# Kernel tuning notes

Measured on AMD Instinct MI355X. Metric: run time of the kernel, lower is better.

## Reference

```python
import jax, jax.numpy as jnp
import numpy as np

HEAD_SIZE = 64
EMBED = 512


def setup_inputs() -> dict:
    key = jax.random.key(0)
    kx, kk, kq, kv = jax.random.split(key, 4)
    x = jax.random.normal(kx, (4, 4096, EMBED), dtype=jnp.float32)
    # torch Linear(EMBED, HEAD_SIZE, bias=False) weight: [HEAD_SIZE, EMBED]
    scale = 1.0 / np.sqrt(EMBED)
    Wk = jax.random.normal(kk, (HEAD_SIZE, EMBED), dtype=jnp.float32) * scale
    Wq = jax.random.normal(kq, (HEAD_SIZE, EMBED), dtype=jnp.float32) * scale
    Wv = jax.random.normal(kv, (HEAD_SIZE, EMBED), dtype=jnp.float32) * scale
    return {"x": x, "Wk": Wk, "Wq": Wq, "Wv": Wv}


def reference(x, Wk, Wq, Wv):
    B, T, C = x.shape
    # projections: x @ W.T  -> [B, T, H]
    k = jnp.einsum('btc,hc->bth', x, Wk)
    q = jnp.einsum('btc,hc->bth', x, Wq)
    v = jnp.einsum('btc,hc->bth', x, Wv)
    # scores scaled by C**-0.5 (input embed dim, as in the source module)
    scores = jnp.einsum('bth,bsh->bts', q, k) * (C ** -0.5)  # [B, T, T]
    causal = jnp.tril(jnp.ones((T, T), dtype=bool))
    scores = jnp.where(causal, scores, -jnp.inf)
    weights = jax.nn.softmax(scores, axis=-1)
    # dropout p=0.0 -> identity
    out = jnp.einsum('bts,bsh->bth', weights, v)  # [B, T, H]
    return out
```

## Files before the change

kernel.cpp:

```cpp
#include <hip/hip_runtime.h>

typedef unsigned short u16;
typedef unsigned int   u32;

#define NB 4
#define NT 4096
#define NC 512
#define NH 64
#define ATT_SCALE 0.044194173824159216f
#define LOG2E     1.4426950408889634f
#define QSCALE    (ATT_SCALE * LOG2E)
#define NEG_BIG   -30000.0f
#define ITEMS3_PB 288

typedef __attribute__((ext_vector_type(8))) _Float16 half8;
typedef __attribute__((ext_vector_type(4))) _Float16 half4;
typedef __attribute__((ext_vector_type(4))) float    floatx4;

__device__ __forceinline__ void gld16(const void* g, void* l) {
    __builtin_amdgcn_global_load_lds(
        (const __attribute__((address_space(1))) void*)g,
        (__attribute__((address_space(3))) void*)l, 16, 0, 0);
}


__global__ __launch_bounds__(256) void wconv(
    const float* __restrict__ Wk, const float* __restrict__ Wq,
    const float* __restrict__ Wv, _Float16* __restrict__ Wh)
{
    const int gid = blockIdx.x * 256 + threadIdx.x;
    const int w = gid >> 13;
    const int i = gid & 8191;
    const int h = i >> 7, c = (i & 127) * 4;
    const float* src = (w == 0) ? Wq : (w == 1) ? Wk : Wv;
    const float sc = (w == 0) ? QSCALE : 1.0f;
    float4 f = *(const float4*)&src[h * NC + c];
    half4 o = {(_Float16)(f.x * sc), (_Float16)(f.y * sc),
               (_Float16)(f.z * sc), (_Float16)(f.w * sc)};
    const int blk = ((w * 16 + (c >> 5)) * 4 + (h >> 4));
    *(half4*)&Wh[(size_t)blk * 512 + (h & 15) * 32 + ((c >> 3) & 3) * 8 + (c & 7)] = o;
}

__global__ __launch_bounds__(256) void qkv_mfma(
    const float* __restrict__ x, const _Float16* __restrict__ Wh,
    _Float16* __restrict__ Qf, _Float16* __restrict__ Kf,
    _Float16* __restrict__ Vf)
{
    __shared__ __align__(16) _Float16 Ws[2][12 * 512];
    __shared__ __align__(16) float    Xs[3][64 * 32];

    const int tid  = threadIdx.x;
    const int wv   = tid >> 6;
    const int lane = tid & 63;
    const int quad = lane >> 4;
    const int id   = lane & 15;
    const int loff = id * 32 + quad * 8;
    const int rowbase = blockIdx.x * 64;

    const int xrow  = wv * 16 + (lane >> 3);
    const int xchk  = (lane & 7) ^ ((lane >> 3) & 7);
    const float* xs0 = x + (size_t)(rowbase + xrow) * NC + xchk * 4;
    const float* xs1 = xs0 + 8 * NC;

    floatx4 acc[3][4] = {};

    gld16(xs0, &Xs[0][wv * 512]);
    gld16(xs1, &Xs[0][wv * 512 + 256]);
#pragma unroll
    for (int jj = 0; jj < 3; ++jj) {
        const int f = 3 * wv + jj;
        gld16(Wh + (size_t)(((f >> 2) * 16 + 0) * 4 + (f & 3)) * 512 + loff,
              &Ws[0][f * 512]);
    }
    gld16(xs0 + 32, &Xs[1][wv * 512]);
    gld16(xs1 + 32, &Xs[1][wv * 512 + 256]);

    int xcur = 0;
    for (int s = 0; s < 16; ++s) {
        if (s + 2 < 16) asm volatile("s_waitcnt vmcnt(2)" ::: "memory");
        else            asm volatile("s_waitcnt vmcnt(0)" ::: "memory");
        __syncthreads();

        if (s + 1 < 16) {
            _Float16* wdst = &Ws[(s + 1) & 1][0];
#pragma unroll
            for (int jj = 0; jj < 3; ++jj) {
                const int f = 3 * wv + jj;
                gld16(Wh + (size_t)(((f >> 2) * 16 + (s + 1)) * 4 + (f & 3)) * 512 + loff,
                      wdst + f * 512);
            }
        }
        if (s + 2 < 16) {
            const int nb = (xcur + 2 >= 3) ? xcur - 1 : xcur + 2;
            float* xdst = &Xs[nb][wv * 512];
            gld16(xs0 + (s + 2) * 32, xdst);
            gld16(xs1 + (s + 2) * 32, xdst + 256);
        }

        const float* Xc = &Xs[xcur][wv * 512 + id * 32];
        float4 f0 = *(const float4*)&Xc[((quad * 2 + 0) ^ (id & 7)) << 2];
        float4 f1 = *(const float4*)&Xc[((quad * 2 + 1) ^ (id & 7)) << 2];
        half8 a;
        a[0] = (_Float16)f0.x; a[1] = (_Float16)f0.y;
        a[2] = (_Float16)f0.z; a[3] = (_Float16)f0.w;
        a[4] = (_Float16)f1.x; a[5] = (_Float16)f1.y;
        a[6] = (_Float16)f1.z; a[7] = (_Float16)f1.w;

        const _Float16* Wc = &Ws[s & 1][0];
#pragma unroll
        for (int f = 0; f < 12; ++f) {
            half8 bf = *(const half8*)&Wc[f * 512 + lane * 8];
            acc[f >> 2][f & 3] = __builtin_amdgcn_mfma_f32_16x16x32_f16(a, bf, acc[f >> 2][f & 3], 0, 0, 0);
        }
        xcur = (xcur + 1 == 3) ? 0 : xcur + 1;
    }

    const int rowb = rowbase + wv * 16;
    const int b2 = rowb >> 12, L = rowb & 4095;
    const int q16 = L >> 4, ktt = L >> 6, tt = (L >> 4) & 3;
    const int kop = ((rowb & 63) + quad * 4) >> 5;
    const int q4k = (((rowb & 63) + quad * 4) >> 3) & 3;
#pragma unroll
    for (int nt = 0; nt < 4; ++nt) {
        const int hop = nt >> 1;
        const int q4h = (nt * 2 + (id >> 3)) & 3;
        const int j   = id & 7;
        const size_t qa2 = (size_t)((b2 * 256 + q16) * 2 + hop) * 512 + q4h * 8 + j;
        const size_t ka2 = (size_t)(((b2 * 64 + ktt) * 4 + tt) * 2 + hop) * 512 + q4h * 8 + j;
#pragma unroll
        for (int r = 0; r < 4; ++r) {
            Qf[qa2 + (quad * 4 + r) * 32] = (_Float16)acc[0][nt][r];
            Kf[ka2 + (quad * 4 + r) * 32] = (_Float16)acc[1][nt][r];
        }
        half4 vh = {(_Float16)acc[2][nt][0], (_Float16)acc[2][nt][1],
                    (_Float16)acc[2][nt][2], (_Float16)acc[2][nt][3]};
        const size_t va2 = (size_t)(((b2 * 64 + ktt) * 4 + nt) * 2 + kop) * 512
                         + id * 32 + q4k * 8 + (quad & 1) * 4;
        *(half4*)&Vf[va2] = vh;
    }
}

__global__ __launch_bounds__(256) void attn_part(
    const _Float16* __restrict__ Qf, const _Float16* __restrict__ Kf,
    const _Float16* __restrict__ Vf, _Float16* __restrict__ Opart,
    float2* __restrict__ MLpart)
{
    constexpr int KP = 72;
    __shared__ __align__(16) _Float16 KV[2][2][4096];
    __shared__ __align__(16) _Float16 Ps[4][16 * KP];

    const int tid  = threadIdx.x;
    const int wv   = tid >> 6;
    const int lane = tid & 63;
    const int quad = lane >> 4;
    const int id   = lane & 15;
    const int b    = blockIdx.y;
    const int item = (ITEMS3_PB - 1) - blockIdx.x;
    const int loff = id * 32 + quad * 8;

    int g = (int)(0.5f * (__builtin_sqrtf((float)item + 1.0f) - 1.0f));
    while (4 * (g + 1) * (g + 2) <= item) ++g;
    while (g > 0 && 4 * g * (g + 1) > item) --g;
    const int rem = item - 4 * g * (g + 1);
    const int np  = g + 1;
    const int qb  = 8 * g + rem / np;
    const int seg = rem - (rem / np) * np;
    const int ntl = qb + 1;
    const int t0 = seg * ntl / np, t1 = (seg + 1) * ntl / np;

    const size_t qa = (size_t)((b * 256 + qb * 4 + wv) * 2) * 512 + loff;
    const half8 qb0 = *(const half8*)&Qf[qa];
    const half8 qb1 = *(const half8*)&Qf[qa + 512];

    size_t gk = (size_t)((b * 64 + t0) * 8) * 512;
    const int c0 = 2 * wv, c1 = 2 * wv + 1;

#define STAGE4(GBASE, BUF) do {                                              \
    gld16(&Kf[(GBASE) + (size_t)c0 * 512 + loff], &KV[BUF][0][c0 * 512]);    \
    gld16(&Kf[(GBASE) + (size_t)c1 * 512 + loff], &KV[BUF][0][c1 * 512]);    \
    gld16(&Vf[(GBASE) + (size_t)c0 * 512 + loff], &KV[BUF][1][c0 * 512]);    \
    gld16(&Vf[(GBASE) + (size_t)c1 * 512 + loff], &KV[BUF][1][c1 * 512]);    \
} while (0)

    STAGE4(gk, 0);
    if (t0 + 1 < t1) STAGE4(gk + 4096, 1);

    floatx4 o[4] = {};
    float m_i = NEG_BIG;
    float l_q = 0.f;

    int cur = 0;
    for (int kt = t0; kt < t1; ++kt) {
        if (kt + 1 < t1) asm volatile("s_waitcnt vmcnt(4)" ::: "memory");
        else             asm volatile("s_waitcnt vmcnt(0)" ::: "memory");
        __syncthreads();

        const _Float16* Kc = &KV[cur][0][0];
        const _Float16* Vc = &KV[cur][1][0];

        floatx4 s4[4] = {};
        __builtin_amdgcn_s_setprio(1);
#pragma unroll
        for (int t = 0; t < 4; ++t) {
            const half8 k0 = *(const half8*)&Kc[(size_t)(2 * t)     * 512 + lane * 8];
            const half8 k1 = *(const half8*)&Kc[(size_t)(2 * t + 1) * 512 + lane * 8];
            s4[t] = __builtin_amdgcn_mfma_f32_16x16x32_f16(k0, qb0, s4[t], 0, 0, 0);
            s4[t] = __builtin_amdgcn_mfma_f32_16x16x32_f16(k1, qb1, s4[t], 0, 0, 0);
        }
        __builtin_amdgcn_s_setprio(0);

        if (kt == qb) {
            const int qrow = wv * 16 + id;
#pragma unroll
            for (int t = 0; t < 4; ++t)
#pragma unroll
                for (int r = 0; r < 4; ++r)
                    if (16 * t + quad * 4 + r > qrow)
                        s4[t][r] = NEG_BIG;
        }

        half8 vf[8];
#pragma unroll
        for (int c = 0; c < 8; ++c)
            vf[c] = *(const half8*)&Vc[(size_t)c * 512 + lane * 8];

        float pmax = s4[0][0];
#pragma unroll
        for (int t = 0; t < 4; ++t)
#pragma unroll
            for (int r = 0; r < 4; ++r) pmax = fmaxf(pmax, s4[t][r]);

        if (__any(pmax > m_i + 8.0f)) {
            float mx = pmax;
            mx = fmaxf(mx, __shfl_xor(mx, 16));
            mx = fmaxf(mx, __shfl_xor(mx, 32));
            const float mnew  = fmaxf(m_i, mx);
            const float alpha = exp2f(m_i - mnew);
            m_i = mnew;
            l_q *= alpha;
#pragma unroll
            for (int t = 0; t < 4; ++t)
#pragma unroll
                for (int r = 0; r < 4; ++r) o[t][r] *= alpha;
        }

        float psum = 0.f;
#pragma unroll
        for (int t = 0; t < 4; ++t)
#pragma unroll
            for (int r = 0; r < 4; ++r) {
                const float p = exp2f(s4[t][r] - m_i);
                s4[t][r] = p;
                psum += p;
            }
        l_q += psum;

#pragma unroll
        for (int t = 0; t < 4; ++t) {
            half4 ph = {(_Float16)s4[t][0], (_Float16)s4[t][1],
                        (_Float16)s4[t][2], (_Float16)s4[t][3]};
            *(half4*)&Ps[wv][id * KP + 16 * t + quad * 4] = ph;
        }
        const half8 pb0 = *(const half8*)&Ps[wv][id * KP + quad * 8];
        const half8 pb1 = *(const half8*)&Ps[wv][id * KP + 32 + quad * 8];

        __builtin_amdgcn_s_setprio(1);
#pragma unroll
        for (int t = 0; t < 4; ++t) {
            o[t] = __builtin_amdgcn_mfma_f32_16x16x32_f16(vf[2 * t],     pb0, o[t], 0, 0, 0);
            o[t] = __builtin_amdgcn_mfma_f32_16x16x32_f16(vf[2 * t + 1], pb1, o[t], 0, 0, 0);
        }
        __builtin_amdgcn_s_setprio(0);

        __syncthreads();
        if (kt + 2 < t1)
            STAGE4(gk + 2 * 4096, cur);
        cur ^= 1;
        gk += 4096;
    }
#undef STAGE4

    float l_t = l_q;
    l_t += __shfl_xor(l_t, 16);
    l_t += __shfl_xor(l_t, 32);

    const int p = b * ITEMS3_PB + item;
    const float rl = 1.f / l_t;
#pragma unroll
    for (int t = 0; t < 4; ++t) {
        half4 oh = {(_Float16)(o[t][0] * rl), (_Float16)(o[t][1] * rl),
                    (_Float16)(o[t][2] * rl), (_Float16)(o[t][3] * rl)};
        *(half4*)&Ps[wv][id * KP + 16 * t + quad * 4] = oh;
    }
    const int rr = lane >> 3, rc = (lane & 7) * 8;
    half8 u0 = *(const half8*)&Ps[wv][rr * KP + rc];
    half8 u1 = *(const half8*)&Ps[wv][(8 + rr) * KP + rc];
    _Float16* ob = &Opart[((size_t)p * 64 + wv * 16) * NH];
    *(half8*)&ob[rr * NH + rc] = u0;
    *(half8*)&ob[(8 + rr) * NH + rc] = u1;

    if (quad == 0)
        MLpart[(size_t)p * 64 + wv * 16 + id] = make_float2(m_i, l_t);
}

__global__ __launch_bounds__(256) void attn_combine(
    const _Float16* __restrict__ Opart, const float2* __restrict__ MLpart,
    float* __restrict__ out)
{
    const int b   = blockIdx.y;
    const int tid = threadIdx.x;
    const int row = blockIdx.x * 32 + (tid >> 3);
    const int hc  = tid & 7;
    const int qb  = row >> 6;
    const int rin = row & 63;
    const int g   = qb >> 3;
    const int m   = g + 1;
    const int base = 4 * g * (g + 1) + (qb & 7) * m;

    auto gidx = [&](int k) -> size_t {
        return ((size_t)b * ITEMS3_PB + base + k) * 64 + rin;
    };

    float2 ml[8];
#pragma unroll
    for (int k = 0; k < 8; ++k)
        ml[k] = MLpart[gidx(k < m ? k : 0)];

    half8 ohv[8];
#pragma unroll
    for (int k = 0; k < 8; ++k)
        ohv[k] = *(const half8*)&Opart[gidx(k < m ? k : 0) * NH + hc * 8];

    float M = NEG_BIG;
#pragma unroll
    for (int k = 0; k < 8; ++k)
        if (k < m) M = fmaxf(M, ml[k].x);

    float w[8], W = 0.f;
#pragma unroll
    for (int k = 0; k < 8; ++k) {
        const float wk = (k < m) ? ml[k].y * exp2f(ml[k].x - M) : 0.f;
        w[k] = wk; W += wk;
    }

    float acc[8] = {};
#pragma unroll
    for (int k = 0; k < 8; ++k)
#pragma unroll
        for (int j = 0; j < 8; ++j) acc[j] += w[k] * (float)ohv[k][j];

    const float rl = 1.f / W;
    float* dst = out + (size_t)(b * NT + row) * NH + hc * 8;
#pragma unroll
    for (int j = 0; j < 8; ++j) dst[j] = acc[j] * rl;
}

extern "C" void kernel_launch(void* const* d_in, const int* in_sizes, int n_in,
                              void* d_out, int out_size, void* d_ws, size_t ws_size,
                              hipStream_t stream) {
    const float* x  = (const float*)d_in[0];
    const float* Wk = (const float*)d_in[1];
    const float* Wq = (const float*)d_in[2];
    const float* Wv = (const float*)d_in[3];

    char* wsb = (char*)d_ws;
    _Float16* Qf    = (_Float16*)wsb;
    _Float16* Kf    = Qf + 1048576;
    _Float16* Vf    = Kf + 1048576;
    _Float16* Wh    = Vf + 1048576;
    float2*   MLpart= (float2*)(wsb + 6488064);
    _Float16* Opart = (_Float16*)(wsb + 7602176);

    wconv<<<96, 256, 0, stream>>>(Wk, Wq, Wv, Wh);
    qkv_mfma<<<256, 256, 0, stream>>>(x, Wh, Qf, Kf, Vf);
    attn_part<<<dim3(ITEMS3_PB, NB), 256, 0, stream>>>(Qf, Kf, Vf, Opart, MLpart);
    attn_combine<<<dim3(128, NB), 256, 0, stream>>>(Opart, MLpart, (float*)d_out);
}
```

Before: 122.5 us.

## Load V straight to registers, stage only K in LDS, use fast exp

```diff
diff --git a/kernel.cpp b/kernel.cpp
--- a/kernel.cpp
+++ b/kernel.cpp
@@ -15,12 +15,19 @@
 
 typedef __attribute__((ext_vector_type(8))) _Float16 half8;
 typedef __attribute__((ext_vector_type(4))) _Float16 half4;
+typedef __attribute__((ext_vector_type(2))) _Float16 h2_t;
 typedef __attribute__((ext_vector_type(4))) float    floatx4;
 
 __device__ __forceinline__ void gld16(const void* g, void* l) {
     __builtin_amdgcn_global_load_lds(
         (const __attribute__((address_space(1))) void*)g,
         (__attribute__((address_space(3))) void*)l, 16, 0, 0);
+}
+
+__device__ __forceinline__ float exp2_fast(float x) {
+    float r;
+    asm volatile("v_exp_f32 %0, %1\n\ts_nop 1" : "=v"(r) : "v"(x));
+    return r;
 }
 
 
@@ -77,9 +84,10 @@
 
     int xcur = 0;
     for (int s = 0; s < 16; ++s) {
-        if (s + 2 < 16) asm volatile("s_waitcnt vmcnt(2)" ::: "memory");
+        if (s + 1 < 16) asm volatile("s_waitcnt vmcnt(2)" ::: "memory");
         else            asm volatile("s_waitcnt vmcnt(0)" ::: "memory");
-        __syncthreads();
+        __builtin_amdgcn_s_barrier();
+        asm volatile("" ::: "memory");
 
         if (s + 1 < 16) {
             _Float16* wdst = &Ws[(s + 1) & 1][0];
@@ -140,13 +148,13 @@
     }
 }
 
-__global__ __launch_bounds__(256) void attn_part(
+__global__ __launch_bounds__(256, 4) void attn_part(
     const _Float16* __restrict__ Qf, const _Float16* __restrict__ Kf,
     const _Float16* __restrict__ Vf, _Float16* __restrict__ Opart,
     float2* __restrict__ MLpart)
 {
     constexpr int KP = 72;
-    __shared__ __align__(16) _Float16 KV[2][2][4096];
+    __shared__ __align__(16) _Float16 Ks[2][4096];
     __shared__ __align__(16) _Float16 Ps[4][16 * KP];
 
     const int tid  = threadIdx.x;
@@ -175,15 +183,13 @@
     size_t gk = (size_t)((b * 64 + t0) * 8) * 512;
     const int c0 = 2 * wv, c1 = 2 * wv + 1;
 
-#define STAGE4(GBASE, BUF) do {                                              \
-    gld16(&Kf[(GBASE) + (size_t)c0 * 512 + loff], &KV[BUF][0][c0 * 512]);    \
-    gld16(&Kf[(GBASE) + (size_t)c1 * 512 + loff], &KV[BUF][0][c1 * 512]);    \
-    gld16(&Vf[(GBASE) + (size_t)c0 * 512 + loff], &KV[BUF][1][c0 * 512]);    \
-    gld16(&Vf[(GBASE) + (size_t)c1 * 512 + loff], &KV[BUF][1][c1 * 512]);    \
+#define STAGE2(GBASE, BUF) do {                                              \
+    gld16(&Kf[(GBASE) + (size_t)c0 * 512 + loff], &Ks[BUF][c0 * 512]);       \
+    gld16(&Kf[(GBASE) + (size_t)c1 * 512 + loff], &Ks[BUF][c1 * 512]);       \
 } while (0)
 
-    STAGE4(gk, 0);
-    if (t0 + 1 < t1) STAGE4(gk + 4096, 1);
+    STAGE2(gk, 0);
+    if (t0 + 1 < t1) STAGE2(gk + 4096, 1);
 
     floatx4 o[4] = {};
     float m_i = NEG_BIG;
@@ -191,12 +197,12 @@
 
     int cur = 0;
     for (int kt = t0; kt < t1; ++kt) {
-        if (kt + 1 < t1) asm volatile("s_waitcnt vmcnt(4)" ::: "memory");
+        if (kt + 1 < t1) asm volatile("s_waitcnt vmcnt(2)" ::: "memory");
         else             asm volatile("s_waitcnt vmcnt(0)" ::: "memory");
-        __syncthreads();
-
-        const _Float16* Kc = &KV[cur][0][0];
-        const _Float16* Vc = &KV[cur][1][0];
+        __builtin_amdgcn_s_barrier();
+        asm volatile("" ::: "memory");
+
+        const _Float16* Kc = &Ks[cur][0];
 
         floatx4 s4[4] = {};
         __builtin_amdgcn_s_setprio(1);
@@ -209,6 +215,11 @@
         }
         __builtin_amdgcn_s_setprio(0);
 
+        half8 vf[8];
+#pragma unroll
+        for (int c = 0; c < 8; ++c)
+            vf[c] = *(const half8*)&Vf[gk + (size_t)c * 512 + loff];
+
         if (kt == qb) {
             const int qrow = wv * 16 + id;
 #pragma unroll
@@ -219,23 +230,18 @@
                         s4[t][r] = NEG_BIG;
         }
 
-        half8 vf[8];
-#pragma unroll
-        for (int c = 0; c < 8; ++c)
-            vf[c] = *(const half8*)&Vc[(size_t)c * 512 + lane * 8];
-
-        float pmax = s4[0][0];
-#pragma unroll
-        for (int t = 0; t < 4; ++t)
-#pragma unroll
-            for (int r = 0; r < 4; ++r) pmax = fmaxf(pmax, s4[t][r]);
+        float a0 = fmaxf(fmaxf(s4[0][0], s4[0][1]), fmaxf(s4[0][2], s4[0][3]));
+        float a1 = fmaxf(fmaxf(s4[1][0], s4[1][1]), fmaxf(s4[1][2], s4[1][3]));
+        float a2 = fmaxf(fmaxf(s4[2][0], s4[2][1]), fmaxf(s4[2][2], s4[2][3]));
+        float a3 = fmaxf(fmaxf(s4[3][0], s4[3][1]), fmaxf(s4[3][2], s4[3][3]));
+        const float pmax = fmaxf(fmaxf(a0, a1), fmaxf(a2, a3));
 
         if (__any(pmax > m_i + 8.0f)) {
             float mx = pmax;
             mx = fmaxf(mx, __shfl_xor(mx, 16));
             mx = fmaxf(mx, __shfl_xor(mx, 32));
             const float mnew  = fmaxf(m_i, mx);
-            const float alpha = exp2f(m_i - mnew);
+            const float alpha = exp2_fast(m_i - mnew);
             m_i = mnew;
             l_q *= alpha;
 #pragma unroll
@@ -246,21 +252,19 @@
 
         float psum = 0.f;
 #pragma unroll
-        for (int t = 0; t < 4; ++t)
-#pragma unroll
-            for (int r = 0; r < 4; ++r) {
-                const float p = exp2f(s4[t][r] - m_i);
-                s4[t][r] = p;
-                psum += p;
-            }
+        for (int t = 0; t < 4; ++t) {
+            const float p0 = exp2_fast(s4[t][0] - m_i);
+            const float p1 = exp2_fast(s4[t][1] - m_i);
+            const float p2 = exp2_fast(s4[t][2] - m_i);
+            const float p3 = exp2_fast(s4[t][3] - m_i);
+            psum += (p0 + p1) + (p2 + p3);
+            const h2_t lo = __builtin_bit_cast(h2_t, __builtin_amdgcn_cvt_pkrtz(p0, p1));
+            const h2_t hi = __builtin_bit_cast(h2_t, __builtin_amdgcn_cvt_pkrtz(p2, p3));
+            half4 ph; ph.x = lo.x; ph.y = lo.y; ph.z = hi.x; ph.w = hi.y;
+            *(half4*)&Ps[wv][id * KP + 16 * t + quad * 4] = ph;
+        }
         l_q += psum;
 
-#pragma unroll
-        for (int t = 0; t < 4; ++t) {
-            half4 ph = {(_Float16)s4[t][0], (_Float16)s4[t][1],
-                        (_Float16)s4[t][2], (_Float16)s4[t][3]};
-            *(half4*)&Ps[wv][id * KP + 16 * t + quad * 4] = ph;
-        }
         const half8 pb0 = *(const half8*)&Ps[wv][id * KP + quad * 8];
         const half8 pb1 = *(const half8*)&Ps[wv][id * KP + 32 + quad * 8];
 
@@ -272,13 +276,15 @@
         }
         __builtin_amdgcn_s_setprio(0);
 
-        __syncthreads();
+        asm volatile("" ::: "memory");
+        __builtin_amdgcn_s_barrier();
+        asm volatile("" ::: "memory");
         if (kt + 2 < t1)
-            STAGE4(gk + 2 * 4096, cur);
+            STAGE2(gk + 2 * 4096, cur);
         cur ^= 1;
         gk += 4096;
     }
-#undef STAGE4
+#undef STAGE2
 
     float l_t = l_q;
     l_t += __shfl_xor(l_t, 16);
```

Measured after the change: 124.1 us. About the same (+1.3%).
